# Optimization experiments

Hardware: AMD Instinct MI355X
Metric: run time of the kernel (lower is better)

## Reference

```python
import jax, jax.numpy as jnp
import numpy as np

B, D, H, L = 2048, 4096, 1024, 64
LAM = 1.0  # topo_lambda


def setup_inputs() -> dict:
    key = jax.random.key(0)
    ks = jax.random.split(key, 5)
    def w(k, sh):
        fan_in = sh[0]
        return (jax.random.normal(k, sh, jnp.float32) * (1.0 / fan_in) ** 0.5)
    return {
        "x": jax.random.normal(ks[0], (B, D), jnp.float32),
        "W1": w(ks[1], (D, H)), "b1": jnp.zeros((H,), jnp.float32),
        "W2": w(ks[2], (H, L)), "b2": jnp.zeros((L,), jnp.float32),
        "W3": w(ks[3], (L, H)), "b3": jnp.zeros((H,), jnp.float32),
        "W4": w(ks[4], (H, D)), "b4": jnp.zeros((D,), jnp.float32),
        "latent_norm": jnp.ones((1,), jnp.float32),
    }


def _cdist(a):
    # pairwise euclidean distances [N, N], safe sqrt (zero grad on zero diag)
    sq = jnp.sum(a * a, axis=1)
    d2 = jnp.maximum(sq[:, None] + sq[None, :] - 2.0 * (a @ a.T), 0.0)
    pos = d2 > 0
    return jnp.where(pos, jnp.sqrt(jnp.where(pos, d2, 1.0)), 0.0)


def _mst_edges(d):
    # 0-dim persistence pairs == MST edges of the dense distance matrix.
    # Vectorized Prim's algorithm: scan of N-1 steps, O(N) work per step.
    n = d.shape[0]
    in_tree = jnp.zeros((n,), bool).at[0].set(True)
    min_dist = d[0]
    parent = jnp.zeros((n,), jnp.int32)

    def step(carry, _):
        in_tree, min_dist, parent = carry
        j = jnp.argmin(jnp.where(in_tree, jnp.inf, min_dist)).astype(jnp.int32)
        i = parent[j]
        in_tree = in_tree.at[j].set(True)
        better = (d[j] < min_dist) & ~in_tree
        min_dist = jnp.where(better, d[j], min_dist)
        parent = jnp.where(better, j, parent)
        return (in_tree, min_dist, parent), jnp.stack([i, j])

    _, edges = jax.lax.scan(step, (in_tree, min_dist, parent), None, length=n - 1)
    return edges  # [n-1, 2] int32


def _topo_signature(dx, dz):
    # pairing indices computed on detached distances (as in torch .detach())
    p1 = _mst_edges(jax.lax.stop_gradient(dx))
    p2 = _mst_edges(jax.lax.stop_gradient(dz))
    sig1 = dx[p1[:, 0], p1[:, 1]]
    sig1_2 = dz[p1[:, 0], p1[:, 1]]
    sig2 = dz[p2[:, 0], p2[:, 1]]
    sig2_1 = dx[p2[:, 0], p2[:, 1]]
    # match_edges == 'symmetric'
    return jnp.sum((sig1 - sig1_2) ** 2) + jnp.sum((sig2 - sig2_1) ** 2)


def reference(x, W1, b1, W2, b2, W3, b3, W4, b4, latent_norm):
    z = jax.nn.relu(x @ W1 + b1) @ W2 + b2            # [B, L]
    x_rec = jax.nn.relu(z @ W3 + b3) @ W4 + b4        # [B, D]
    rec_loss = jnp.mean((x_rec - x) ** 2)
    x_dist = _cdist(x)
    x_dist = x_dist / jnp.max(x_dist)
    z_dist = _cdist(z) / latent_norm[0]
    topo_loss = _topo_signature(x_dist, z_dist) / x.shape[0]
    loss = rec_loss + LAM * topo_loss
    return loss
```

## Files before the change

kernel.cpp:

```cpp
#include <hip/hip_runtime.h>
#include <hip/hip_bf16.h>

#define B_N 2048
#define D_N 4096
#define H_N 1024
#define L_N 64

typedef __attribute__((ext_vector_type(8))) short short8;
typedef __attribute__((ext_vector_type(4))) float float4_t;

#define ASG __attribute__((address_space(1)))
#define ASL __attribute__((address_space(3)))

__device__ inline float bf2f(unsigned short u) {
  union { unsigned u; float f; } v; v.u = ((unsigned)u) << 16; return v.f;
}
__device__ inline unsigned short f2bf(float f) {
  union { float f; unsigned u; } v; v.f = f;
  unsigned r = v.u + 0x7fffu + ((v.u >> 16) & 1u);
  return (unsigned short)(r >> 16);
}

__device__ inline float block_sum256(float v) {
  const int lane = threadIdx.x & 63, wave = threadIdx.x >> 6;
#pragma unroll
  for (int off = 32; off; off >>= 1) v += __shfl_xor(v, off);
  __shared__ float red_s[4];
  if (lane == 0) red_s[wave] = v;
  __syncthreads();
  return red_s[0] + red_s[1] + red_s[2] + red_s[3];
}

__device__ inline float block_max256(float v) {
  const int lane = threadIdx.x & 63, wave = threadIdx.x >> 6;
#pragma unroll
  for (int off = 32; off; off >>= 1) v = fmaxf(v, __shfl_xor(v, off));
  __shared__ float redm_s[4];
  if (lane == 0) redm_s[wave] = v;
  __syncthreads();
  return fmaxf(fmaxf(redm_s[0], redm_s[1]), fmaxf(redm_s[2], redm_s[3]));
}


__global__ __launch_bounds__(256) void prep_x(const float* __restrict__ x,
                                              unsigned short* __restrict__ xb,
                                              float* __restrict__ sqx) {
  const int row = blockIdx.x;
  const int t = threadIdx.x;
  const float4* xr = (const float4*)(x + (size_t)row * D_N);
  ushort4* xbr = (ushort4*)(xb + (size_t)row * D_N);
  float s = 0.f;
  for (int i = t; i < D_N / 4; i += 256) {
    float4 v = xr[i];
    s += v.x * v.x + v.y * v.y + v.z * v.z + v.w * v.w;
    ushort4 o;
    o.x = f2bf(v.x); o.y = f2bf(v.y); o.z = f2bf(v.z); o.w = f2bf(v.w);
    xbr[i] = o;
  }
  float tot = block_sum256(s);
  if (t == 0) sqx[row] = tot;
}

__global__ __launch_bounds__(256) void transpose_cast(const float* __restrict__ in,
                                                      unsigned short* __restrict__ out,
                                                      int R, int C) {
  __shared__ float tile[32][33];
  const int c0 = blockIdx.x * 32, r0 = blockIdx.y * 32;
  const int tx = threadIdx.x, ty = threadIdx.y;
#pragma unroll
  for (int i = 0; i < 32; i += 8)
    tile[ty + i][tx] = in[(size_t)(r0 + ty + i) * C + c0 + tx];
  __syncthreads();
#pragma unroll
  for (int i = 0; i < 32; i += 8)
    out[(size_t)(c0 + ty + i) * R + r0 + tx] = f2bf(tile[tx][ty + i]);
}

__global__ __launch_bounds__(1024) void init_bor(float* __restrict__ accum,
                                                 int* __restrict__ comp,
                                                 unsigned long long* __restrict__ best,
                                                 int* __restrict__ cnt,
                                                 int* __restrict__ done) {
  const int t = threadIdx.x;
  if (t < 2) { accum[t] = 0.f; cnt[t] = 0; done[t] = 0; }
  for (int v = t; v < 2 * B_N; v += 1024) {
    comp[v] = v & (B_N - 1);
    best[v] = ~0ull;
  }
}


__device__ inline void gemm_mainloop(const unsigned short* __restrict__ A,
                                     const unsigned short* __restrict__ Bt,
                                     int ld, int Klen, int m_base, int n_base,
                                     float4_t acc[4][4]) {
  __shared__ unsigned short lA[128 * 32];
  __shared__ unsigned short lB[128 * 32];
  const int t = threadIdx.x;
  const int wave = t >> 6;
  const int lane = t & 63;
  const int lrow = lane & 15;
  const int quad = lane >> 4;
  const int wm = (wave & 1) * 64;
  const int wn = (wave >> 1) * 64;

  const int srow = lane >> 2;
  const int scol = (lane & 3) * 8;

  for (int k0 = 0; k0 < Klen; k0 += 32) {
    __syncthreads();
#pragma unroll
    for (int q = 0; q < 2; ++q) {
      const int rbase = wave * 32 + q * 16;
      const int row = rbase + srow;
      __builtin_amdgcn_global_load_lds(
          (ASG void*)(A + (size_t)(m_base + row) * ld + k0 + scol),
          (ASL void*)(lA + rbase * 32), 16, 0, 0);
      __builtin_amdgcn_global_load_lds(
          (ASG void*)(Bt + (size_t)(n_base + row) * ld + k0 + scol),
          (ASL void*)(lB + rbase * 32), 16, 0, 0);
    }
    __syncthreads();
    short8 af[4], bfr[4];
#pragma unroll
    for (int f = 0; f < 4; ++f) {
      af[f]  = *(const short8*)(lA + (wm + f * 16 + lrow) * 32 + quad * 8);
      bfr[f] = *(const short8*)(lB + (wn + f * 16 + lrow) * 32 + quad * 8);
    }
#pragma unroll
    for (int fm = 0; fm < 4; ++fm)
#pragma unroll
      for (int fn = 0; fn < 4; ++fn)
        acc[fm][fn] = __builtin_amdgcn_mfma_f32_16x16x32_bf16(af[fm], bfr[fn],
                                                              acc[fm][fn], 0, 0, 0);
  }
}

__global__ __launch_bounds__(256) void gemm_splitk(const unsigned short* __restrict__ A,
                                                   const unsigned short* __restrict__ Bt,
                                                   int ld, int Kchunk, int N,
                                                   float* __restrict__ partial) {
  float4_t acc[4][4];
  float4_t z4 = {0.f, 0.f, 0.f, 0.f};
#pragma unroll
  for (int a = 0; a < 4; ++a)
#pragma unroll
    for (int b = 0; b < 4; ++b) acc[a][b] = z4;
  const int s = blockIdx.z;
  const int m_base = blockIdx.y * 128, n_base = blockIdx.x * 128;
  gemm_mainloop(A + (size_t)s * Kchunk, Bt + (size_t)s * Kchunk, ld, Kchunk,
                m_base, n_base, acc);
  const size_t MN = (size_t)gridDim.y * 128 * N;
  float* __restrict__ P = partial + (size_t)s * MN;
  const int t = threadIdx.x, wave = t >> 6, lane = t & 63;
  const int lrow = lane & 15, quad = lane >> 4;
  const int wm = (wave & 1) * 64, wn = (wave >> 1) * 64;
#pragma unroll
  for (int fm = 0; fm < 4; ++fm)
#pragma unroll
    for (int fn = 0; fn < 4; ++fn) {
      const int r0 = m_base + wm + fm * 16 + quad * 4;
      const int c = n_base + wn + fn * 16 + lrow;
#pragma unroll
      for (int r = 0; r < 4; ++r)
        P[(size_t)(r0 + r) * N + c] = acc[fm][fn][r];
    }
}

__global__ __launch_bounds__(256) void fin_bias_relu(const float* __restrict__ partial,
                                                     const float* __restrict__ bias,
                                                     unsigned short* __restrict__ out) {
  const size_t MN = (size_t)B_N * H_N;
  const size_t i4 = ((size_t)blockIdx.x * 256 + threadIdx.x) * 4;
  float4 a = *(const float4*)(partial + i4);
#pragma unroll
  for (int s = 1; s < 4; ++s) {
    float4 p = *(const float4*)(partial + s * MN + i4);
    a.x += p.x; a.y += p.y; a.z += p.z; a.w += p.w;
  }
  const int c = (int)(i4 & (H_N - 1));
  float4 b = *(const float4*)(bias + c);
  ushort4 o;
  o.x = f2bf(fmaxf(a.x + b.x, 0.f));
  o.y = f2bf(fmaxf(a.y + b.y, 0.f));
  o.z = f2bf(fmaxf(a.z + b.z, 0.f));
  o.w = f2bf(fmaxf(a.w + b.w, 0.f));
  *(ushort4*)(out + i4) = o;
}

__global__ __launch_bounds__(256) void fin_d2(const float* __restrict__ partial,
                                              const float* __restrict__ sq,
                                              float* __restrict__ Out,
                                              unsigned* __restrict__ max_slot) {
  const size_t MN = (size_t)B_N * B_N;
  const size_t i4 = ((size_t)blockIdx.x * 256 + threadIdx.x) * 4;
  float4 a = *(const float4*)(partial + i4);
#pragma unroll
  for (int s = 1; s < 4; ++s) {
    float4 p = *(const float4*)(partial + s * MN + i4);
    a.x += p.x; a.y += p.y; a.z += p.z; a.w += p.w;
  }
  const int i = (int)(i4 >> 11);
  const int j = (int)(i4 & (B_N - 1));
  const float si = sq[i];
  float4 sj = *(const float4*)(sq + j);
  float4 v;
  v.x = fmaxf(si + sj.x - 2.f * a.x, 0.f);
  v.y = fmaxf(si + sj.y - 2.f * a.y, 0.f);
  v.z = fmaxf(si + sj.z - 2.f * a.z, 0.f);
  v.w = fmaxf(si + sj.w - 2.f * a.w, 0.f);
  *(float4*)(Out + i4) = v;
  float lmax = fmaxf(fmaxf(v.x, v.y), fmaxf(v.z, v.w));
  float tot = block_max256(lmax);
  if (threadIdx.x == 0) atomicMax(max_slot, __float_as_uint(tot));
}

__global__ __launch_bounds__(256) void gemm_recloss(const unsigned short* __restrict__ A,
                                                    const unsigned short* __restrict__ Bt,
                                                    const float* __restrict__ bias,
                                                    const float* __restrict__ Xref,
                                                    float* __restrict__ acc_slot,
                                                    int K, int N) {
  float4_t acc[4][4];
  float4_t z4 = {0.f, 0.f, 0.f, 0.f};
#pragma unroll
  for (int a = 0; a < 4; ++a)
#pragma unroll
    for (int b = 0; b < 4; ++b) acc[a][b] = z4;
  const int m_base = blockIdx.y * 128, n_base = blockIdx.x * 128;
  gemm_mainloop(A, Bt, K, K, m_base, n_base, acc);
  const int t = threadIdx.x, wave = t >> 6, lane = t & 63;
  const int lrow = lane & 15, quad = lane >> 4;
  const int wm = (wave & 1) * 64, wn = (wave >> 1) * 64;
  float local = 0.f;
#pragma unroll
  for (int fm = 0; fm < 4; ++fm)
#pragma unroll
    for (int fn = 0; fn < 4; ++fn) {
      const int r0 = m_base + wm + fm * 16 + quad * 4;
      const int c = n_base + wn + fn * 16 + lrow;
      const float bc = bias[c];
#pragma unroll
      for (int r = 0; r < 4; ++r) {
        float v = acc[fm][fn][r] + bc - Xref[(size_t)(r0 + r) * N + c];
        local += v * v;
      }
    }
  float tot = block_sum256(local);
  if (t == 0) atomicAdd(acc_slot, tot);
}


__global__ __launch_bounds__(256) void g2_k(const unsigned short* __restrict__ h1b,
                                            const float* __restrict__ W2,
                                            const float* __restrict__ b2,
                                            float* __restrict__ z) {
  const int col = threadIdx.x & 63;
  const int row = blockIdx.x * 4 + (threadIdx.x >> 6);
  const unsigned short* hr = h1b + (size_t)row * H_N;
  float a0 = 0.f, a1 = 0.f, a2 = 0.f, a3 = 0.f;
  for (int k = 0; k < H_N; k += 4) {
    a0 += bf2f(hr[k + 0]) * W2[(k + 0) * L_N + col];
    a1 += bf2f(hr[k + 1]) * W2[(k + 1) * L_N + col];
    a2 += bf2f(hr[k + 2]) * W2[(k + 2) * L_N + col];
    a3 += bf2f(hr[k + 3]) * W2[(k + 3) * L_N + col];
  }
  z[(size_t)row * L_N + col] = (a0 + a1) + (a2 + a3) + b2[col];
}

__global__ __launch_bounds__(256) void sqz_k(const float* __restrict__ z,
                                             float* __restrict__ sqz) {
  const int lane = threadIdx.x & 63;
  const int row = blockIdx.x * 4 + (threadIdx.x >> 6);
  float v = z[(size_t)row * L_N + lane];
  float s = v * v;
#pragma unroll
  for (int off = 32; off; off >>= 1) s += __shfl_xor(s, off);
  if (lane == 0) sqz[row] = s;
}

__global__ __launch_bounds__(256) void g3_k(const float* __restrict__ z,
                                            const float* __restrict__ W3,
                                            const float* __restrict__ b3,
                                            unsigned short* __restrict__ h2b) {
  const int t = threadIdx.x;
  const int col = blockIdx.y * 256 + t;
  const int r0 = blockIdx.x * 4;
  __shared__ float zr[4][64];
  zr[t >> 6][t & 63] = z[(size_t)(r0 + (t >> 6)) * L_N + (t & 63)];
  __syncthreads();
  const float bc = b3[col];
  float a0 = bc, a1 = bc, a2 = bc, a3 = bc;
#pragma unroll 8
  for (int k = 0; k < 64; ++k) {
    float w = W3[k * H_N + col];
    a0 += zr[0][k] * w;
    a1 += zr[1][k] * w;
    a2 += zr[2][k] * w;
    a3 += zr[3][k] * w;
  }
  h2b[(size_t)(r0 + 0) * H_N + col] = f2bf(fmaxf(a0, 0.f));
  h2b[(size_t)(r0 + 1) * H_N + col] = f2bf(fmaxf(a1, 0.f));
  h2b[(size_t)(r0 + 2) * H_N + col] = f2bf(fmaxf(a2, 0.f));
  h2b[(size_t)(r0 + 3) * H_N + col] = f2bf(fmaxf(a3, 0.f));
}

__global__ __launch_bounds__(256) void d2z_k(const float* __restrict__ z,
                                             const float* __restrict__ sqz,
                                             float* __restrict__ d2z) {
  const int bi = blockIdx.y * 16, bj = blockIdx.x * 16;
  __shared__ float zi[16][65], zj[16][65];
  const int t = threadIdx.x;
  for (int idx = t; idx < 16 * 64; idx += 256) {
    const int r = idx >> 6, c = idx & 63;
    zi[r][c] = z[(size_t)(bi + r) * L_N + c];
    zj[r][c] = z[(size_t)(bj + r) * L_N + c];
  }
  __syncthreads();
  const int ti = t >> 4, tj = t & 15;
  float dot = 0.f;
#pragma unroll 8
  for (int k = 0; k < 64; ++k) dot += zi[ti][k] * zj[tj][k];
  float v = fmaxf(sqz[bi + ti] + sqz[bj + tj] - 2.f * dot, 0.f);
  d2z[(size_t)(bi + ti) * B_N + bj + tj] = v;
}


__global__ __launch_bounds__(256) void bor_scan(const float* __restrict__ d2x,
                                                const float* __restrict__ d2z,
                                                const int* __restrict__ comp,
                                                unsigned long long* __restrict__ best,
                                                const int* __restrict__ done) {
  const int tree = blockIdx.y;
  if (done[tree]) return;
  const float* __restrict__ d2 = tree ? d2z : d2x;
  const int* __restrict__ cp = comp + tree * B_N;
  unsigned long long* __restrict__ bst = best + tree * B_N;
  const int i = blockIdx.x;
  const int t = threadIdx.x;
  const int ci = cp[i];
  const float* __restrict__ row = d2 + (size_t)i * B_N;
  const unsigned ibase = (unsigned)(i << 11);
  unsigned long long k = ~0ull;
#pragma unroll
  for (int m = 0; m < 2; ++m) {
    const int j4 = (t + m * 256) * 4;
    float4 dv = *(const float4*)(row + j4);
    int4 cj = *(const int4*)(cp + j4);
    if (cj.x != ci) {
      unsigned long long key = (((unsigned long long)__float_as_uint(dv.x)) << 32) | (ibase | (unsigned)(j4 + 0));
      k = key < k ? key : k;
    }
    if (cj.y != ci) {
      unsigned long long key = (((unsigned long long)__float_as_uint(dv.y)) << 32) | (ibase | (unsigned)(j4 + 1));
      k = key < k ? key : k;
    }
    if (cj.z != ci) {
      unsigned long long key = (((unsigned long long)__float_as_uint(dv.z)) << 32) | (ibase | (unsigned)(j4 + 2));
      k = key < k ? key : k;
    }
    if (cj.w != ci) {
      unsigned long long key = (((unsigned long long)__float_as_uint(dv.w)) << 32) | (ibase | (unsigned)(j4 + 3));
      k = key < k ? key : k;
    }
  }
  const int lane = t & 63, wave = t >> 6;
#pragma unroll
  for (int off = 32; off; off >>= 1) {
    unsigned long long o = __shfl_xor(k, off);
    k = o < k ? o : k;
  }
  __shared__ unsigned long long wmin[4];
  if (lane == 0) wmin[wave] = k;
  __syncthreads();
  if (t == 0) {
    unsigned long long a = wmin[0] < wmin[1] ? wmin[0] : wmin[1];
    unsigned long long b = wmin[2] < wmin[3] ? wmin[2] : wmin[3];
    k = a < b ? a : b;
    if (k != ~0ull) atomicMin(bst + ci, k);
  }
}

__global__ __launch_bounds__(1024) void bor_merge(unsigned long long* __restrict__ best,
                                                  int* __restrict__ comp,
                                                  int2* __restrict__ edges,
                                                  int* __restrict__ cnt,
                                                  int* __restrict__ done) {
  const int tree = blockIdx.x;
  if (done[tree]) return;
  unsigned long long* __restrict__ bst = best + tree * B_N;
  int* __restrict__ cp = comp + tree * B_N;
  int2* __restrict__ eo = edges + (size_t)tree * (B_N - 1);
  int* __restrict__ cn = cnt + tree;
  __shared__ int hk[B_N];
  __shared__ int allsame;
  const int t = threadIdx.x;

  unsigned long long mykey[2];
#pragma unroll
  for (int q = 0; q < 2; ++q) {
    const int c = t + q * 1024;
    unsigned long long key = bst[c];
    mykey[q] = key;
    int h = c;
    if (key != ~0ull) h = cp[(unsigned)key & (unsigned)(B_N - 1)];
    hk[c] = h;
  }
  __syncthreads();

  int rloc[2];
#pragma unroll
  for (int q = 0; q < 2; ++q) {
    const int c = t + q * 1024;
    const unsigned long long key = mykey[q];
    const int h = hk[c];
    const int hh = hk[h];
    const bool valid = key != ~0ull;
    const bool two = (h != c) && (hh == c);
    rloc[q] = (two && c < h) ? c : h;
    if (valid && (!two || c < h)) {
      int e = atomicAdd(cn, 1);
      eo[e] = make_int2((int)((key >> 11) & (unsigned)(B_N - 1)),
                        (int)(key & (unsigned)(B_N - 1)));
    }
    bst[c] = ~0ull;
  }
  __syncthreads();
#pragma unroll
  for (int q = 0; q < 2; ++q) hk[t + q * 1024] = rloc[q];
  if (t == 0) allsame = 1;
  __syncthreads();

  for (int it = 0; it < 11; ++it) {
    const int v0 = hk[hk[t]];
    const int v1 = hk[hk[t + 1024]];
    __syncthreads();
    hk[t] = v0;
    hk[t + 1024] = v1;
    __syncthreads();
  }

#pragma unroll
  for (int q = 0; q < 2; ++q) {
    const int v = t + q * 1024;
    cp[v] = hk[cp[v]];
  }
  __syncthreads();

  const int c0 = cp[0];
  if (cp[t] != c0 || cp[t + 1024] != c0) allsame = 0;
  __syncthreads();
  if (t == 0 && allsame) done[tree] = 1;
}

__global__ __launch_bounds__(256) void final_k(const float* __restrict__ d2x,
                                               const float* __restrict__ d2z,
                                               const int2* __restrict__ edges,
                                               const float* __restrict__ accum,
                                               const float* __restrict__ latent_norm,
                                               float* __restrict__ out) {
  const int t = threadIdx.x;
  const float maxd = sqrtf(__uint_as_float(((const unsigned*)accum)[1]));
  const float inv_maxd = 1.0f / maxd;
  const float inv_ln = 1.0f / latent_norm[0];
  float local = 0.f;
  for (int e = t; e < 2 * (B_N - 1); e += 256) {
    int2 ij = edges[e];
    size_t idx = (size_t)ij.x * B_N + ij.y;
    float xd = sqrtf(d2x[idx]) * inv_maxd;
    float zd = sqrtf(d2z[idx]) * inv_ln;
    float d = xd - zd;
    local += d * d;
  }
  float topo = block_sum256(local);
  if (t == 0)
    out[0] = accum[0] * (1.0f / ((float)B_N * (float)D_N)) + topo * (1.0f / (float)B_N);
}

extern "C" void kernel_launch(void* const* d_in, const int* in_sizes, int n_in,
                              void* d_out, int out_size, void* d_ws, size_t ws_size,
                              hipStream_t stream) {
  const float* x  = (const float*)d_in[0];
  const float* W1 = (const float*)d_in[1];
  const float* b1 = (const float*)d_in[2];
  const float* W2 = (const float*)d_in[3];
  const float* b2 = (const float*)d_in[4];
  const float* W3 = (const float*)d_in[5];
  const float* b3 = (const float*)d_in[6];
  const float* W4 = (const float*)d_in[7];
  const float* b4 = (const float*)d_in[8];
  const float* latent_norm = (const float*)d_in[9];
  float* out = (float*)d_out;

  char* ws = (char*)d_ws;
  size_t off = 0;
  auto alloc = [&](size_t bytes) {
    size_t o = off;
    off += (bytes + 255) & ~(size_t)255;
    return o;
  };
  unsigned short* xb   = (unsigned short*)(ws + alloc((size_t)B_N * D_N * 2));
  unsigned short* w1bt = (unsigned short*)(ws + alloc((size_t)H_N * D_N * 2));
  unsigned short* w4bt = (unsigned short*)(ws + alloc((size_t)D_N * H_N * 2));
  unsigned short* h1b  = (unsigned short*)(ws + alloc((size_t)B_N * H_N * 2));
  unsigned short* h2b  = (unsigned short*)(ws + alloc((size_t)B_N * H_N * 2));
  float* z    = (float*)(ws + alloc((size_t)B_N * L_N * 4));
  float* sqx  = (float*)(ws + alloc((size_t)B_N * 4));
  float* sqz  = (float*)(ws + alloc((size_t)B_N * 4));
  float* d2x  = (float*)(ws + alloc((size_t)B_N * B_N * 4));
  float* d2z  = (float*)(ws + alloc((size_t)B_N * B_N * 4));
  int2* edges = (int2*)(ws + alloc((size_t)2 * (B_N - 1) * sizeof(int2)));
  float* accum = (float*)(ws + alloc(256));
  int* comp   = (int*)(ws + alloc((size_t)2 * B_N * 4));
  unsigned long long* best = (unsigned long long*)(ws + alloc((size_t)2 * B_N * 8));
  int* cnt    = (int*)(ws + alloc(256));
  int* done   = (int*)(ws + alloc(256));
  float* parts = (float*)(ws + alloc((size_t)4 * B_N * B_N * 4));

  init_bor<<<1, 1024, 0, stream>>>(accum, comp, best, cnt, done);
  prep_x<<<B_N, 256, 0, stream>>>(x, xb, sqx);
  transpose_cast<<<dim3(H_N / 32, D_N / 32), dim3(32, 8), 0, stream>>>(W1, w1bt, D_N, H_N);
  transpose_cast<<<dim3(D_N / 32, H_N / 32), dim3(32, 8), 0, stream>>>(W4, w4bt, H_N, D_N);

  gemm_splitk<<<dim3(H_N / 128, B_N / 128, 4), 256, 0, stream>>>(xb, w1bt, D_N, D_N / 4,
                                                                 H_N, parts);
  fin_bias_relu<<<(B_N * H_N) / 1024, 256, 0, stream>>>(parts, b1, h1b);

  g2_k<<<B_N / 4, 256, 0, stream>>>(h1b, W2, b2, z);
  sqz_k<<<B_N / 4, 256, 0, stream>>>(z, sqz);
  g3_k<<<dim3(B_N / 4, H_N / 256), 256, 0, stream>>>(z, W3, b3, h2b);
  gemm_recloss<<<dim3(D_N / 128, B_N / 128), 256, 0, stream>>>(h2b, w4bt, b4, x, accum, H_N, D_N);

  gemm_splitk<<<dim3(B_N / 128, B_N / 128, 4), 256, 0, stream>>>(xb, xb, D_N, D_N / 4,
                                                                 B_N, parts);
  fin_d2<<<(B_N * B_N) / 1024, 256, 0, stream>>>(parts, sqx, d2x, (unsigned*)(accum + 1));

  d2z_k<<<dim3(B_N / 16, B_N / 16), 256, 0, stream>>>(z, sqz, d2z);

  for (int r = 0; r < 11; ++r) {
    bor_scan<<<dim3(B_N, 2), 256, 0, stream>>>(d2x, d2z, comp, best, done);
    bor_merge<<<2, 1024, 0, stream>>>(best, comp, edges, cnt, done);
  }
  final_k<<<1, 256, 0, stream>>>(d2x, d2z, edges, accum, latent_norm, out);
}
```

Measured before the change: 478.6 us.

## Exploit Gram symmetry, fuse sqz into g2, merge Boruvka scan and merge via last-block

The x Gram matrix GEMM now computes only the lower-triangular 128x128 tiles (136 of 256), and a new finalize kernel writes each tile and its transpose through LDS, roughly halving the split-K MMA work and partial traffic. The squared-norm kernel for z is folded into g2_k. Each Boruvka round is now one kernel: the last block to finish, found through an atomic counter, performs the component merge, which removes 11 launches. The cost is a serialized 256-thread merge tail in one block and transposed writes whose coalescing depends on the LDS staging.

```diff
diff --git a/kernel.cpp b/kernel.cpp
--- a/kernel.cpp
+++ b/kernel.cpp
@@ -5,6 +5,7 @@
 #define D_N 4096
 #define H_N 1024
 #define L_N 64
+#define NTILE 136
 
 typedef __attribute__((ext_vector_type(8))) short short8;
 typedef __attribute__((ext_vector_type(4))) float float4_t;
@@ -39,6 +40,14 @@
   if (lane == 0) redm_s[wave] = v;
   __syncthreads();
   return fmaxf(fmaxf(redm_s[0], redm_s[1]), fmaxf(redm_s[2], redm_s[3]));
+}
+
+__device__ inline void tri_idx(int b, int& tm, int& tn) {
+  int m = (int)((sqrtf(8.f * (float)b + 1.f) - 1.f) * 0.5f);
+  while ((m + 1) * (m + 2) / 2 <= b) ++m;
+  while (m * (m + 1) / 2 > b) --m;
+  tm = m;
+  tn = b - m * (m + 1) / 2;
 }
 
 
@@ -80,9 +89,10 @@
                                                  int* __restrict__ comp,
                                                  unsigned long long* __restrict__ best,
                                                  int* __restrict__ cnt,
-                                                 int* __restrict__ done) {
-  const int t = threadIdx.x;
-  if (t < 2) { accum[t] = 0.f; cnt[t] = 0; done[t] = 0; }
+                                                 int* __restrict__ done,
+                                                 int* __restrict__ ctr) {
+  const int t = threadIdx.x;
+  if (t < 2) { accum[t] = 0.f; cnt[t] = 0; done[t] = 0; ctr[t] = 0; }
   for (int v = t; v < 2 * B_N; v += 1024) {
     comp[v] = v & (B_N - 1);
     best[v] = ~0ull;
@@ -167,6 +177,35 @@
     }
 }
 
+__global__ __launch_bounds__(256) void gemm_d2_tri(const unsigned short* __restrict__ xb,
+                                                   float* __restrict__ partial) {
+  float4_t acc[4][4];
+  float4_t z4 = {0.f, 0.f, 0.f, 0.f};
+#pragma unroll
+  for (int a = 0; a < 4; ++a)
+#pragma unroll
+    for (int b = 0; b < 4; ++b) acc[a][b] = z4;
+  const int s = blockIdx.z;
+  int tm, tn;
+  tri_idx(blockIdx.x, tm, tn);
+  gemm_mainloop(xb + (size_t)s * (D_N / 4), xb + (size_t)s * (D_N / 4), D_N, D_N / 4,
+                tm * 128, tn * 128, acc);
+  float* __restrict__ P = partial + ((size_t)s * NTILE + blockIdx.x) * 16384;
+  const int t = threadIdx.x, wave = t >> 6, lane = t & 63;
+  const int lrow = lane & 15, quad = lane >> 4;
+  const int wm = (wave & 1) * 64, wn = (wave >> 1) * 64;
+#pragma unroll
+  for (int fm = 0; fm < 4; ++fm)
+#pragma unroll
+    for (int fn = 0; fn < 4; ++fn) {
+      const int lr0 = wm + fm * 16 + quad * 4;
+      const int lc = wn + fn * 16 + lrow;
+#pragma unroll
+      for (int r = 0; r < 4; ++r)
+        P[(lr0 + r) * 128 + lc] = acc[fm][fn][r];
+    }
+}
+
 __global__ __launch_bounds__(256) void fin_bias_relu(const float* __restrict__ partial,
                                                      const float* __restrict__ bias,
                                                      unsigned short* __restrict__ out) {
@@ -188,31 +227,54 @@
   *(ushort4*)(out + i4) = o;
 }
 
-__global__ __launch_bounds__(256) void fin_d2(const float* __restrict__ partial,
-                                              const float* __restrict__ sq,
-                                              float* __restrict__ Out,
-                                              unsigned* __restrict__ max_slot) {
-  const size_t MN = (size_t)B_N * B_N;
-  const size_t i4 = ((size_t)blockIdx.x * 256 + threadIdx.x) * 4;
-  float4 a = *(const float4*)(partial + i4);
-#pragma unroll
-  for (int s = 1; s < 4; ++s) {
-    float4 p = *(const float4*)(partial + s * MN + i4);
-    a.x += p.x; a.y += p.y; a.z += p.z; a.w += p.w;
-  }
-  const int i = (int)(i4 >> 11);
-  const int j = (int)(i4 & (B_N - 1));
-  const float si = sq[i];
-  float4 sj = *(const float4*)(sq + j);
-  float4 v;
-  v.x = fmaxf(si + sj.x - 2.f * a.x, 0.f);
-  v.y = fmaxf(si + sj.y - 2.f * a.y, 0.f);
-  v.z = fmaxf(si + sj.z - 2.f * a.z, 0.f);
-  v.w = fmaxf(si + sj.w - 2.f * a.w, 0.f);
-  *(float4*)(Out + i4) = v;
-  float lmax = fmaxf(fmaxf(v.x, v.y), fmaxf(v.z, v.w));
+__global__ __launch_bounds__(256) void fin_d2_tri(const float* __restrict__ partial,
+                                                  const float* __restrict__ sq,
+                                                  float* __restrict__ Out,
+                                                  unsigned* __restrict__ max_slot) {
+  const int tile = blockIdx.y;
+  const int c0 = blockIdx.x * 32;
+  int tm, tn;
+  tri_idx(tile, tm, tn);
+  __shared__ float lds[32][132];
+  const int t = threadIdx.x;
+  const int cc = (t & 7) * 4;
+  float lmax = 0.f;
+#pragma unroll
+  for (int q = 0; q < 4; ++q) {
+    const int r = (t >> 3) + 32 * q;
+    const float* base = partial + (size_t)tile * 16384 + r * 128 + c0 + cc;
+    float4 a = *(const float4*)base;
+#pragma unroll
+    for (int s = 1; s < 4; ++s) {
+      float4 p = *(const float4*)(base + (size_t)s * NTILE * 16384);
+      a.x += p.x; a.y += p.y; a.z += p.z; a.w += p.w;
+    }
+    const int i = tm * 128 + r;
+    const float si = sq[i];
+    float4 sj = *(const float4*)(sq + tn * 128 + c0 + cc);
+    float4 v;
+    v.x = fmaxf(si + sj.x - 2.f * a.x, 0.f);
+    v.y = fmaxf(si + sj.y - 2.f * a.y, 0.f);
+    v.z = fmaxf(si + sj.z - 2.f * a.z, 0.f);
+    v.w = fmaxf(si + sj.w - 2.f * a.w, 0.f);
+    *(float4*)(Out + (size_t)i * B_N + tn * 128 + c0 + cc) = v;
+    lds[cc + 0][r] = v.x;
+    lds[cc + 1][r] = v.y;
+    lds[cc + 2][r] = v.z;
+    lds[cc + 3][r] = v.w;
+    lmax = fmaxf(lmax, fmaxf(fmaxf(v.x, v.y), fmaxf(v.z, v.w)));
+  }
+  __syncthreads();
+#pragma unroll
+  for (int m = 0; m < 4; ++m) {
+    const int lin = t + 256 * m;
+    const int cc2 = lin >> 5;
+    const int r4 = (lin & 31) * 4;
+    float4 w = *(const float4*)(&lds[cc2][r4]);
+    *(float4*)(Out + (size_t)(tn * 128 + c0 + cc2) * B_N + tm * 128 + r4) = w;
+  }
   float tot = block_max256(lmax);
-  if (threadIdx.x == 0) atomicMax(max_slot, __float_as_uint(tot));
+  if (t == 0) atomicMax(max_slot, __float_as_uint(tot));
 }
 
 __global__ __launch_bounds__(256) void gemm_recloss(const unsigned short* __restrict__ A,
@@ -254,7 +316,8 @@
 __global__ __launch_bounds__(256) void g2_k(const unsigned short* __restrict__ h1b,
                                             const float* __restrict__ W2,
                                             const float* __restrict__ b2,
-                                            float* __restrict__ z) {
+                                            float* __restrict__ z,
+                                            float* __restrict__ sqz) {
   const int col = threadIdx.x & 63;
   const int row = blockIdx.x * 4 + (threadIdx.x >> 6);
   const unsigned short* hr = h1b + (size_t)row * H_N;
@@ -265,18 +328,12 @@
     a2 += bf2f(hr[k + 2]) * W2[(k + 2) * L_N + col];
     a3 += bf2f(hr[k + 3]) * W2[(k + 3) * L_N + col];
   }
-  z[(size_t)row * L_N + col] = (a0 + a1) + (a2 + a3) + b2[col];
-}
-
-__global__ __launch_bounds__(256) void sqz_k(const float* __restrict__ z,
-                                             float* __restrict__ sqz) {
-  const int lane = threadIdx.x & 63;
-  const int row = blockIdx.x * 4 + (threadIdx.x >> 6);
-  float v = z[(size_t)row * L_N + lane];
-  float s = v * v;
+  const float zv = (a0 + a1) + (a2 + a3) + b2[col];
+  z[(size_t)row * L_N + col] = zv;
+  float s = zv * zv;
 #pragma unroll
   for (int off = 32; off; off >>= 1) s += __shfl_xor(s, off);
-  if (lane == 0) sqz[row] = s;
+  if (col == 0) sqz[row] = s;
 }
 
 __global__ __launch_bounds__(256) void g3_k(const float* __restrict__ z,
@@ -325,16 +382,18 @@
   d2z[(size_t)(bi + ti) * B_N + bj + tj] = v;
 }
 
-
-__global__ __launch_bounds__(256) void bor_scan(const float* __restrict__ d2x,
-                                                const float* __restrict__ d2z,
-                                                const int* __restrict__ comp,
-                                                unsigned long long* __restrict__ best,
-                                                const int* __restrict__ done) {
+__global__ __launch_bounds__(256) void bor_round(const float* __restrict__ d2x,
+                                                 const float* __restrict__ d2z,
+                                                 int* __restrict__ comp,
+                                                 unsigned long long* __restrict__ best,
+                                                 int2* __restrict__ edges,
+                                                 int* __restrict__ cnt,
+                                                 int* __restrict__ done,
+                                                 int* __restrict__ ctr) {
   const int tree = blockIdx.y;
   if (done[tree]) return;
   const float* __restrict__ d2 = tree ? d2z : d2x;
-  const int* __restrict__ cp = comp + tree * B_N;
+  int* __restrict__ cp = comp + tree * B_N;
   unsigned long long* __restrict__ bst = best + tree * B_N;
   const int i = blockIdx.x;
   const int t = threadIdx.x;
@@ -371,6 +430,7 @@
     k = o < k ? o : k;
   }
   __shared__ unsigned long long wmin[4];
+  __shared__ int lastflag;
   if (lane == 0) wmin[wave] = k;
   __syncthreads();
   if (t == 0) {
@@ -378,29 +438,24 @@
     unsigned long long b = wmin[2] < wmin[3] ? wmin[2] : wmin[3];
     k = a < b ? a : b;
     if (k != ~0ull) atomicMin(bst + ci, k);
-  }
-}
-
-__global__ __launch_bounds__(1024) void bor_merge(unsigned long long* __restrict__ best,
-                                                  int* __restrict__ comp,
-                                                  int2* __restrict__ edges,
-                                                  int* __restrict__ cnt,
-                                                  int* __restrict__ done) {
-  const int tree = blockIdx.x;
-  if (done[tree]) return;
-  unsigned long long* __restrict__ bst = best + tree * B_N;
-  int* __restrict__ cp = comp + tree * B_N;
+    __threadfence();
+    const int old = atomicAdd(ctr + tree, 1);
+    lastflag = (old == B_N - 1);
+  }
+  __syncthreads();
+  if (!lastflag) return;
+
+  __threadfence();
+  __shared__ int hk[B_N];
+  __shared__ int allsame;
   int2* __restrict__ eo = edges + (size_t)tree * (B_N - 1);
   int* __restrict__ cn = cnt + tree;
-  __shared__ int hk[B_N];
-  __shared__ int allsame;
-  const int t = threadIdx.x;
-
-  unsigned long long mykey[2];
-#pragma unroll
-  for (int q = 0; q < 2; ++q) {
-    const int c = t + q * 1024;
-    unsigned long long key = bst[c];
+
+  unsigned long long mykey[8];
+#pragma unroll
+  for (int q = 0; q < 8; ++q) {
+    const int c = t + 256 * q;
+    unsigned long long key = atomicMin(bst + c, ~0ull);
     mykey[q] = key;
     int h = c;
     if (key != ~0ull) h = cp[(unsigned)key & (unsigned)(B_N - 1)];
@@ -408,10 +463,10 @@
   }
   __syncthreads();
 
-  int rloc[2];
-#pragma unroll
-  for (int q = 0; q < 2; ++q) {
-    const int c = t + q * 1024;
+  int rloc[8];
+#pragma unroll
+  for (int q = 0; q < 8; ++q) {
+    const int c = t + 256 * q;
     const unsigned long long key = mykey[q];
     const int h = hk[c];
     const int hh = hk[h];
@@ -427,30 +482,35 @@
   }
   __syncthreads();
 #pragma unroll
-  for (int q = 0; q < 2; ++q) hk[t + q * 1024] = rloc[q];
+  for (int q = 0; q < 8; ++q) hk[t + 256 * q] = rloc[q];
   if (t == 0) allsame = 1;
   __syncthreads();
 
   for (int it = 0; it < 11; ++it) {
-    const int v0 = hk[hk[t]];
-    const int v1 = hk[hk[t + 1024]];
+    int v[8];
+#pragma unroll
+    for (int q = 0; q < 8; ++q) v[q] = hk[hk[t + 256 * q]];
     __syncthreads();
-    hk[t] = v0;
-    hk[t + 1024] = v1;
+#pragma unroll
+    for (int q = 0; q < 8; ++q) hk[t + 256 * q] = v[q];
     __syncthreads();
   }
 
 #pragma unroll
-  for (int q = 0; q < 2; ++q) {
-    const int v = t + q * 1024;
+  for (int q = 0; q < 8; ++q) {
+    const int v = t + 256 * q;
     cp[v] = hk[cp[v]];
   }
   __syncthreads();
-
-  const int c0 = cp[0];
-  if (cp[t] != c0 || cp[t + 1024] != c0) allsame = 0;
-  __syncthreads();
-  if (t == 0 && allsame) done[tree] = 1;
+  const int c0v = cp[0];
+#pragma unroll
+  for (int q = 0; q < 8; ++q)
+    if (cp[t + 256 * q] != c0v) allsame = 0;
+  __syncthreads();
+  if (t == 0) {
+    if (allsame) done[tree] = 1;
+    atomicSub(ctr + tree, B_N);
+  }
 }
 
 __global__ __launch_bounds__(256) void final_k(const float* __restrict__ d2x,
@@ -515,9 +575,10 @@
   unsigned long long* best = (unsigned long long*)(ws + alloc((size_t)2 * B_N * 8));
   int* cnt    = (int*)(ws + alloc(256));
   int* done   = (int*)(ws + alloc(256));
-  float* parts = (float*)(ws + alloc((size_t)4 * B_N * B_N * 4));
-
-  init_bor<<<1, 1024, 0, stream>>>(accum, comp, best, cnt, done);
+  int* ctr    = (int*)(ws + alloc(256));
+  float* parts = (float*)(ws + alloc((size_t)4 * NTILE * 16384 * 4 + (size_t)4 * B_N * H_N * 4));
+
+  init_bor<<<1, 1024, 0, stream>>>(accum, comp, best, cnt, done, ctr);
   prep_x<<<B_N, 256, 0, stream>>>(x, xb, sqx);
   transpose_cast<<<dim3(H_N / 32, D_N / 32), dim3(32, 8), 0, stream>>>(W1, w1bt, D_N, H_N);
   transpose_cast<<<dim3(D_N / 32, H_N / 32), dim3(32, 8), 0, stream>>>(W4, w4bt, H_N, D_N);
@@ -526,20 +587,17 @@
                                                                  H_N, parts);
   fin_bias_relu<<<(B_N * H_N) / 1024, 256, 0, stream>>>(parts, b1, h1b);
 
-  g2_k<<<B_N / 4, 256, 0, stream>>>(h1b, W2, b2, z);
-  sqz_k<<<B_N / 4, 256, 0, stream>>>(z, sqz);
+  g2_k<<<B_N / 4, 256, 0, stream>>>(h1b, W2, b2, z, sqz);
   g3_k<<<dim3(B_N / 4, H_N / 256), 256, 0, stream>>>(z, W3, b3, h2b);
   gemm_recloss<<<dim3(D_N / 128, B_N / 128), 256, 0, stream>>>(h2b, w4bt, b4, x, accum, H_N, D_N);
 
-  gemm_splitk<<<dim3(B_N / 128, B_N / 128, 4), 256, 0, stream>>>(xb, xb, D_N, D_N / 4,
-                                                                 B_N, parts);
-  fin_d2<<<(B_N * B_N) / 1024, 256, 0, stream>>>(parts, sqx, d2x, (unsigned*)(accum + 1));
+  gemm_d2_tri<<<dim3(NTILE, 1, 4), 256, 0, stream>>>(xb, parts);
+  fin_d2_tri<<<dim3(4, NTILE), 256, 0, stream>>>(parts, sqx, d2x, (unsigned*)(accum + 1));
 
   d2z_k<<<dim3(B_N / 16, B_N / 16), 256, 0, stream>>>(z, sqz, d2z);
 
-  for (int r = 0; r < 11; ++r) {
-    bor_scan<<<dim3(B_N, 2), 256, 0, stream>>>(d2x, d2z, comp, best, done);
-    bor_merge<<<2, 1024, 0, stream>>>(best, comp, edges, cnt, done);
-  }
+  for (int r = 0; r < 11; ++r)
+    bor_round<<<dim3(B_N, 2), 256, 0, stream>>>(d2x, d2z, comp, best, edges, cnt, done, ctr);
+
   final_k<<<1, 256, 0, stream>>>(d2x, d2z, edges, accum, latent_norm, out);
 }
```

Result: slower. 654.9 us (+36.9%).
